# Performance work log

Measured on AMD Instinct MI355X. Metric: run time of the kernel, lower is better.

Reference implementation:

```python
import jax, jax.numpy as jnp
import numpy as np

B, C, H, W, K, NH = 4, 128, 64, 64, 7, 8
DH = C // NH          # per-head dim
PAD = (K - 1) // 2    # symmetric padding since K is odd


def setup_inputs() -> dict:
    key = jax.random.key(0)
    ks = jax.random.split(key, 9)
    s = 1.0 / np.sqrt(C)
    f32 = jnp.float32
    return {
        "x": jax.random.normal(ks[0], (B, C, H, W), f32),
        "wq": jax.random.normal(ks[1], (C, C), f32) * s,
        "bq": jax.random.normal(ks[2], (C,), f32) * 0.01,
        "wk": jax.random.normal(ks[3], (C, C), f32) * s,
        "bk": jax.random.normal(ks[4], (C,), f32) * 0.01,
        "wv": jax.random.normal(ks[5], (C, C), f32) * s,
        "bv": jax.random.normal(ks[6], (C,), f32) * 0.01,
        "pos_h": jax.random.normal(ks[7], (NH, K), f32) * 0.02,
        "pos_w": jax.random.normal(ks[8], (NH, K), f32) * 0.02,
    }


def _unfold(p):
    # p: [B,C,H+K-1,W+K-1] -> [B,C,H,W,K,K] (KxK neighborhood per pixel),
    # matching torch .unfold(2,K,1).unfold(3,K,1). Loop is over fixed kernel size only.
    p1 = jnp.stack([p[:, :, i:i + H, :] for i in range(K)], axis=-1)      # [B,C,H,W+K-1,K]
    return jnp.stack([p1[:, :, :, j:j + W, :] for j in range(K)], axis=-1)  # [B,C,H,W,K,K]


def reference(x, wq, bq, wk, bk, wv, bv, pos_h, pos_w):
    cx = x  # cx defaults to x in the original module
    pc = jnp.pad(cx, ((0, 0), (0, 0), (PAD, PAD), (PAD, PAD)))
    # 1x1 convs are pointwise channel mixes
    k = jnp.einsum('oc,bchw->bohw', wk, pc) + bk[None, :, None, None]
    v = jnp.einsum('oc,bchw->bohw', wv, pc) + bv[None, :, None, None]
    q = jnp.einsum('oc,bchw->bohw', wq, x) + bq[None, :, None, None]

    ku = _unfold(k).reshape(B, NH, DH, H, W, K, K)
    vu = _unfold(v).reshape(B, NH, DH, H, W, K, K)
    qh = q.reshape(B, NH, DH, H, W)

    # per-pixel logits over KxK neighborhood
    logits = jnp.einsum('bndhw,bndhwij->bnhwij', qh, ku)  # [B,NH,H,W,K,K]
    logits = logits + pos_h[None, :, None, None, :, None] + pos_w[None, :, None, None, None, :]

    weights = jax.nn.softmax(logits.reshape(B, NH, H, W, K * K), axis=-1)
    out = jnp.einsum('bnhwk,bndhwk->bndhw', weights, vu.reshape(B, NH, DH, H, W, K * K))
    return out.reshape(B, C, H, W)
```

## Files before the change

### kernel.cpp

```cpp
#include <hip/hip_runtime.h>
#include <cmath>

constexpr int Bn = 4, Cn = 128, Hn = 64, Wn = 64, Kn = 7, NHn = 8, DHn = 16, PADn = 3;
constexpr int HWn = Hn * Wn;
constexpr int TS = 16;
constexpr int HALO = TS + Kn - 1;
constexpr int DP = 20;
constexpr int SMEM_ELEMS = HALO * HALO * DP;

typedef float f32x4 __attribute__((ext_vector_type(4)));
typedef short short8 __attribute__((ext_vector_type(8)));
typedef unsigned int u32x4 __attribute__((ext_vector_type(4)));

__device__ __forceinline__ unsigned short f32_to_bf16_rne(float f) {
  unsigned u = __float_as_uint(f);
  unsigned r = u + 0x7fffu + ((u >> 16) & 1u);
  return (unsigned short)(r >> 16);
}
__device__ __forceinline__ float bf16_to_f32(unsigned short h) {
  return __uint_as_float(((unsigned)h) << 16);
}

__global__ __launch_bounds__(256)
void conv_w(const float* __restrict__ wq, const float* __restrict__ wk,
            const float* __restrict__ wv, unsigned short* __restrict__ Whl)
{
  const int mat = blockIdx.y;
  const float* W = (mat == 0) ? wq : (mat == 1) ? wk : wv;
  const int i = (blockIdx.x * 256 + threadIdx.x) * 4;
  const f32x4 v = *reinterpret_cast<const f32x4*>(W + i);
  unsigned short h[4], l[4];
#pragma unroll
  for (int j = 0; j < 4; ++j) {
    h[j] = f32_to_bf16_rne(v[j]);
    l[j] = f32_to_bf16_rne(v[j] - bf16_to_f32(h[j]));
  }
  unsigned short* base = Whl + (size_t)mat * 2 * 16384;
  unsigned int hw0 = h[0] | ((unsigned)h[1] << 16), hw1 = h[2] | ((unsigned)h[3] << 16);
  unsigned int lw0 = l[0] | ((unsigned)l[1] << 16), lw1 = l[2] | ((unsigned)l[3] << 16);
  *reinterpret_cast<uint2*>(base + i)          = make_uint2(hw0, hw1);
  *reinterpret_cast<uint2*>(base + 16384 + i)  = make_uint2(lw0, lw1);
}

__global__ __launch_bounds__(256)
void conv_xT(const float* __restrict__ x, unsigned short* __restrict__ xThl)
{
  __shared__ float sm[32][65];
  const int b   = blockIdx.z;
  const int c0g = blockIdx.y * 32;
  const int p0g = blockIdx.x * 64;
  const int t   = threadIdx.x;
  const float* xb = x + (size_t)b * Cn * HWn;

#pragma unroll
  for (int rep = 0; rep < 2; ++rep) {
    const int cl = rep * 16 + (t >> 4);
    const int pl = (t & 15) * 4;
    const f32x4 v = *reinterpret_cast<const f32x4*>(xb + (size_t)(c0g + cl) * HWn + p0g + pl);
    sm[cl][pl + 0] = v[0]; sm[cl][pl + 1] = v[1];
    sm[cl][pl + 2] = v[2]; sm[cl][pl + 3] = v[3];
  }
  __syncthreads();

  const int pl = t >> 2;
  const int c0 = (t & 3) * 8;
  u32x4 hw, lw;
#pragma unroll
  for (int j = 0; j < 4; ++j) {
    const float v0 = sm[c0 + 2 * j][pl];
    const float v1 = sm[c0 + 2 * j + 1][pl];
    const unsigned short h0 = f32_to_bf16_rne(v0);
    const unsigned short h1 = f32_to_bf16_rne(v1);
    const unsigned short l0 = f32_to_bf16_rne(v0 - bf16_to_f32(h0));
    const unsigned short l1 = f32_to_bf16_rne(v1 - bf16_to_f32(h1));
    hw[j] = h0 | ((unsigned)h1 << 16);
    lw[j] = l0 | ((unsigned)l1 << 16);
  }
  unsigned short* dst = xThl + (size_t)b * 2 * HWn * Cn + (size_t)(p0g + pl) * Cn + c0g + c0;
  *reinterpret_cast<u32x4*>(dst)             = hw;
  *reinterpret_cast<u32x4*>(dst + HWn * Cn)  = lw;
}

__global__ __launch_bounds__(64)
void qkv_mfma(const unsigned short* __restrict__ Whl,
              const unsigned short* __restrict__ xThl,
              const float* __restrict__ bq_, const float* __restrict__ bk_,
              const float* __restrict__ bv_,
              float* __restrict__ qo, float* __restrict__ ko, float* __restrict__ vo)
{
  const int z   = blockIdx.z;
  const int mat = z >> 2;
  const int b   = z & 3;
  const float* bias = (mat == 0) ? bq_ : (mat == 1) ? bk_ : bv_;
  float* y = ((mat == 0) ? qo : (mat == 1) ? ko : vo) + (size_t)b * Cn * HWn;

  const int lane = threadIdx.x;
  const int r    = lane & 15;
  const int quad = lane >> 4;
  const int mbase = blockIdx.y * 64;
  const int nbase = blockIdx.x * 64;

  const unsigned short* Wm = Whl  + (size_t)mat * 2 * Cn * Cn;
  const unsigned short* Xb = xThl + (size_t)b   * 2 * HWn * Cn;

  f32x4 acc[4][4] = {};

#pragma unroll
  for (int ks = 0; ks < 4; ++ks) {
    const int kk = ks * 32 + quad * 8;
    short8 Ah[4], Al[4], Bh[4], Bl[4];
#pragma unroll
    for (int mt = 0; mt < 4; ++mt) {
      const unsigned short* p = Wm + (size_t)(mbase + mt * 16 + r) * Cn + kk;
      Ah[mt] = *reinterpret_cast<const short8*>(p);
      Al[mt] = *reinterpret_cast<const short8*>(p + Cn * Cn);
    }
#pragma unroll
    for (int nt = 0; nt < 4; ++nt) {
      const unsigned short* p = Xb + (size_t)(nbase + nt * 16 + r) * Cn + kk;
      Bh[nt] = *reinterpret_cast<const short8*>(p);
      Bl[nt] = *reinterpret_cast<const short8*>(p + HWn * Cn);
    }
#pragma unroll
    for (int mt = 0; mt < 4; ++mt)
#pragma unroll
      for (int nt = 0; nt < 4; ++nt) {
        acc[mt][nt] = __builtin_amdgcn_mfma_f32_16x16x32_bf16(Ah[mt], Bh[nt], acc[mt][nt], 0, 0, 0);
        acc[mt][nt] = __builtin_amdgcn_mfma_f32_16x16x32_bf16(Ah[mt], Bl[nt], acc[mt][nt], 0, 0, 0);
        acc[mt][nt] = __builtin_amdgcn_mfma_f32_16x16x32_bf16(Al[mt], Bh[nt], acc[mt][nt], 0, 0, 0);
      }
  }

#pragma unroll
  for (int mt = 0; mt < 4; ++mt) {
#pragma unroll
    for (int reg = 0; reg < 4; ++reg) {
      const int o = mbase + mt * 16 + quad * 4 + reg;
      const float bi = bias[o];
#pragma unroll
      for (int nt = 0; nt < 4; ++nt)
        y[(size_t)o * HWn + nbase + nt * 16 + r] = acc[mt][nt][reg] + bi;
    }
  }
}

__global__ __launch_bounds__(256)
void sasa_attn(const float* __restrict__ q, const float* __restrict__ k,
               const float* __restrict__ v, const float* __restrict__ bk_,
               const float* __restrict__ bv_, const float* __restrict__ pos_h,
               const float* __restrict__ pos_w, float* __restrict__ out)
{
  extern __shared__ float smem[];
  float* ks = smem;
  float* vs = smem + SMEM_ELEMS;

  const int z  = blockIdx.z;
  const int b  = z >> 3;
  const int n  = z & 7;
  const int h0 = blockIdx.y * TS;
  const int w0 = blockIdx.x * TS;
  const int tid = threadIdx.x;
  const int tx = tid & 15;
  const int ty = tid >> 4;

  const int cbase = n * DHn;
  const size_t plane = (size_t)HWn;
  const float* kb = k + ((size_t)b * Cn + cbase) * plane;
  const float* vb = v + ((size_t)b * Cn + cbase) * plane;

  for (int idx = tid; idx < HALO * HALO * DHn; idx += 256) {
    const int d   = idx / (HALO * HALO);
    const int rem = idx - d * (HALO * HALO);
    const int hh  = rem / HALO;
    const int ww  = rem - hh * HALO;
    const int gh  = h0 + hh - PADn;
    const int gw  = w0 + ww - PADn;
    const bool inb = (gh >= 0) && (gh < Hn) && (gw >= 0) && (gw < Wn);
    const int lidx = (hh * HALO + ww) * DP + d;
    ks[lidx] = inb ? kb[(size_t)d * plane + gh * Wn + gw] : bk_[cbase + d];
    vs[lidx] = inb ? vb[(size_t)d * plane + gh * Wn + gw] : bv_[cbase + d];
  }

  const int h = h0 + ty, w = w0 + tx;
  const float* qb = q + ((size_t)b * Cn + cbase) * plane + (size_t)h * Wn + w;
  float qr[DHn];
#pragma unroll
  for (int d = 0; d < DHn; ++d) qr[d] = qb[(size_t)d * plane];

  __syncthreads();

  float logits[Kn * Kn];
#pragma unroll
  for (int i = 0; i < Kn; ++i) {
    const float ph = pos_h[n * Kn + i];
#pragma unroll
    for (int j = 0; j < Kn; ++j) {
      const float* kp = &ks[((ty + i) * HALO + (tx + j)) * DP];
      const float4 k0 = *reinterpret_cast<const float4*>(kp);
      const float4 k1 = *reinterpret_cast<const float4*>(kp + 4);
      const float4 k2 = *reinterpret_cast<const float4*>(kp + 8);
      const float4 k3 = *reinterpret_cast<const float4*>(kp + 12);
      float acc = qr[0] * k0.x;
      acc = fmaf(qr[1],  k0.y, acc);  acc = fmaf(qr[2],  k0.z, acc);
      acc = fmaf(qr[3],  k0.w, acc);  acc = fmaf(qr[4],  k1.x, acc);
      acc = fmaf(qr[5],  k1.y, acc);  acc = fmaf(qr[6],  k1.z, acc);
      acc = fmaf(qr[7],  k1.w, acc);  acc = fmaf(qr[8],  k2.x, acc);
      acc = fmaf(qr[9],  k2.y, acc);  acc = fmaf(qr[10], k2.z, acc);
      acc = fmaf(qr[11], k2.w, acc);  acc = fmaf(qr[12], k3.x, acc);
      acc = fmaf(qr[13], k3.y, acc);  acc = fmaf(qr[14], k3.z, acc);
      acc = fmaf(qr[15], k3.w, acc);
      logits[i * Kn + j] = acc + ph + pos_w[n * Kn + j];
    }
  }

  float mx = -1e30f;
#pragma unroll
  for (int t = 0; t < Kn * Kn; ++t) mx = fmaxf(mx, logits[t]);
  float sum = 0.0f;
#pragma unroll
  for (int t = 0; t < Kn * Kn; ++t) {
    const float e = __expf(logits[t] - mx);
    logits[t] = e;
    sum += e;
  }
  const float inv = 1.0f / sum;

  float o[DHn] = {};
#pragma unroll
  for (int i = 0; i < Kn; ++i) {
#pragma unroll
    for (int j = 0; j < Kn; ++j) {
      const float wt = logits[i * Kn + j];
      const float* vp = &vs[((ty + i) * HALO + (tx + j)) * DP];
      const float4 v0 = *reinterpret_cast<const float4*>(vp);
      const float4 v1 = *reinterpret_cast<const float4*>(vp + 4);
      const float4 v2 = *reinterpret_cast<const float4*>(vp + 8);
      const float4 v3 = *reinterpret_cast<const float4*>(vp + 12);
      o[0]  = fmaf(wt, v0.x, o[0]);   o[1]  = fmaf(wt, v0.y, o[1]);
      o[2]  = fmaf(wt, v0.z, o[2]);   o[3]  = fmaf(wt, v0.w, o[3]);
      o[4]  = fmaf(wt, v1.x, o[4]);   o[5]  = fmaf(wt, v1.y, o[5]);
      o[6]  = fmaf(wt, v1.z, o[6]);   o[7]  = fmaf(wt, v1.w, o[7]);
      o[8]  = fmaf(wt, v2.x, o[8]);   o[9]  = fmaf(wt, v2.y, o[9]);
      o[10] = fmaf(wt, v2.z, o[10]);  o[11] = fmaf(wt, v2.w, o[11]);
      o[12] = fmaf(wt, v3.x, o[12]);  o[13] = fmaf(wt, v3.y, o[13]);
      o[14] = fmaf(wt, v3.z, o[14]);  o[15] = fmaf(wt, v3.w, o[15]);
    }
  }

  float* ob = out + ((size_t)b * Cn + cbase) * plane + (size_t)h * Wn + w;
#pragma unroll
  for (int d = 0; d < DHn; ++d) ob[(size_t)d * plane] = o[d] * inv;
}

extern "C" void kernel_launch(void* const* d_in, const int* in_sizes, int n_in,
                              void* d_out, int out_size, void* d_ws, size_t ws_size,
                              hipStream_t stream) {
  const float* x     = (const float*)d_in[0];
  const float* wq    = (const float*)d_in[1];
  const float* bq    = (const float*)d_in[2];
  const float* wk    = (const float*)d_in[3];
  const float* bk    = (const float*)d_in[4];
  const float* wv    = (const float*)d_in[5];
  const float* bv    = (const float*)d_in[6];
  const float* pos_h = (const float*)d_in[7];
  const float* pos_w = (const float*)d_in[8];
  float* out = (float*)d_out;

  const size_t tensor_elems = (size_t)Bn * Cn * HWn;
  float* q = (float*)d_ws;
  float* k = q + tensor_elems;
  float* v = k + tensor_elems;
  unsigned short* Whl  = (unsigned short*)(v + tensor_elems);
  unsigned short* xThl = Whl + (size_t)3 * 2 * Cn * Cn;

  dim3 gw(16, 3, 1);
  conv_w<<<gw, 256, 0, stream>>>(wq, wk, wv, Whl);

  dim3 gx(HWn / 64, Cn / 32, Bn);
  conv_xT<<<gx, 256, 0, stream>>>(x, xThl);

  dim3 g1(HWn / 64, Cn / 64, 3 * Bn);
  qkv_mfma<<<g1, 64, 0, stream>>>(Whl, xThl, bq, bk, bv, q, k, v);

  dim3 g2(Wn / TS, Hn / TS, Bn * NHn);
  const size_t smem_bytes = 2 * SMEM_ELEMS * sizeof(float);
  sasa_attn<<<g2, 256, smem_bytes, stream>>>(q, k, v, bk, bv, pos_h, pos_w, out);
}
```

Baseline: 132.9 us.

## Store K/V as bf16 in head-pixel-major layout and merge prep kernels

The QKV GEMM epilogue now writes Q as fp32 and K/V as bf16 in a [B,NH,HW,DH] layout. This lets the attention kernel fill its halo tiles with 16-byte vector loads instead of strided scalar gathers, and halves the K/V global traffic and shared-memory footprint. The weight and x conversion kernels are merged into one launch to save a launch. Storing K/V in bf16 lowers their precision, which may hurt accuracy against the fp32 reference.

```diff
diff --git a/kernel.cpp b/kernel.cpp
--- a/kernel.cpp
+++ b/kernel.cpp
@@ -5,12 +5,15 @@
 constexpr int HWn = Hn * Wn;
 constexpr int TS = 16;
 constexpr int HALO = TS + Kn - 1;
-constexpr int DP = 20;
-constexpr int SMEM_ELEMS = HALO * HALO * DP;
+constexpr int NPIX = HALO * HALO;
+constexpr int PSTRIDE_U16 = 24;
+constexpr int PSTRIDE_U32 = 12;
 
 typedef float f32x4 __attribute__((ext_vector_type(4)));
 typedef short short8 __attribute__((ext_vector_type(8)));
 typedef unsigned int u32x4 __attribute__((ext_vector_type(4)));
+typedef unsigned short u16x4 __attribute__((ext_vector_type(4)));
+typedef unsigned short u16x8 __attribute__((ext_vector_type(8)));
 
 __device__ __forceinline__ unsigned short f32_to_bf16_rne(float f) {
   unsigned u = __float_as_uint(f);
@@ -20,36 +23,41 @@
 __device__ __forceinline__ float bf16_to_f32(unsigned short h) {
   return __uint_as_float(((unsigned)h) << 16);
 }
+__device__ __forceinline__ float bflo(unsigned u) { return __uint_as_float(u << 16); }
+__device__ __forceinline__ float bfhi(unsigned u) { return __uint_as_float(u & 0xffff0000u); }
 
 __global__ __launch_bounds__(256)
-void conv_w(const float* __restrict__ wq, const float* __restrict__ wk,
-            const float* __restrict__ wv, unsigned short* __restrict__ Whl)
+void prep(const float* __restrict__ x,
+          const float* __restrict__ wq, const float* __restrict__ wk,
+          const float* __restrict__ wv,
+          unsigned short* __restrict__ Whl, unsigned short* __restrict__ xThl)
 {
-  const int mat = blockIdx.y;
-  const float* W = (mat == 0) ? wq : (mat == 1) ? wk : wv;
-  const int i = (blockIdx.x * 256 + threadIdx.x) * 4;
-  const f32x4 v = *reinterpret_cast<const f32x4*>(W + i);
-  unsigned short h[4], l[4];
-#pragma unroll
-  for (int j = 0; j < 4; ++j) {
-    h[j] = f32_to_bf16_rne(v[j]);
-    l[j] = f32_to_bf16_rne(v[j] - bf16_to_f32(h[j]));
-  }
-  unsigned short* base = Whl + (size_t)mat * 2 * 16384;
-  unsigned int hw0 = h[0] | ((unsigned)h[1] << 16), hw1 = h[2] | ((unsigned)h[3] << 16);
-  unsigned int lw0 = l[0] | ((unsigned)l[1] << 16), lw1 = l[2] | ((unsigned)l[3] << 16);
-  *reinterpret_cast<uint2*>(base + i)          = make_uint2(hw0, hw1);
-  *reinterpret_cast<uint2*>(base + 16384 + i)  = make_uint2(lw0, lw1);
-}
-
-__global__ __launch_bounds__(256)
-void conv_xT(const float* __restrict__ x, unsigned short* __restrict__ xThl)
-{
+  const int t = threadIdx.x;
+  if (blockIdx.z == 4) {
+    if (blockIdx.y != 0 || blockIdx.x >= 48) return;
+    const int mat = blockIdx.x >> 4;
+    const int chunk = blockIdx.x & 15;
+    const float* W = (mat == 0) ? wq : (mat == 1) ? wk : wv;
+    const int i = (chunk * 256 + t) * 4;
+    const f32x4 v = *reinterpret_cast<const f32x4*>(W + i);
+    unsigned short h[4], l[4];
+#pragma unroll
+    for (int j = 0; j < 4; ++j) {
+      h[j] = f32_to_bf16_rne(v[j]);
+      l[j] = f32_to_bf16_rne(v[j] - bf16_to_f32(h[j]));
+    }
+    unsigned short* base = Whl + (size_t)mat * 2 * 16384;
+    *reinterpret_cast<uint2*>(base + i) =
+        make_uint2(h[0] | ((unsigned)h[1] << 16), h[2] | ((unsigned)h[3] << 16));
+    *reinterpret_cast<uint2*>(base + 16384 + i) =
+        make_uint2(l[0] | ((unsigned)l[1] << 16), l[2] | ((unsigned)l[3] << 16));
+    return;
+  }
+
   __shared__ float sm[32][65];
   const int b   = blockIdx.z;
   const int c0g = blockIdx.y * 32;
   const int p0g = blockIdx.x * 64;
-  const int t   = threadIdx.x;
   const float* xb = x + (size_t)b * Cn * HWn;
 
 #pragma unroll
@@ -77,8 +85,8 @@
     lw[j] = l0 | ((unsigned)l1 << 16);
   }
   unsigned short* dst = xThl + (size_t)b * 2 * HWn * Cn + (size_t)(p0g + pl) * Cn + c0g + c0;
-  *reinterpret_cast<u32x4*>(dst)             = hw;
-  *reinterpret_cast<u32x4*>(dst + HWn * Cn)  = lw;
+  *reinterpret_cast<u32x4*>(dst)            = hw;
+  *reinterpret_cast<u32x4*>(dst + HWn * Cn) = lw;
 }
 
 __global__ __launch_bounds__(64)
@@ -86,13 +94,13 @@
               const unsigned short* __restrict__ xThl,
               const float* __restrict__ bq_, const float* __restrict__ bk_,
               const float* __restrict__ bv_,
-              float* __restrict__ qo, float* __restrict__ ko, float* __restrict__ vo)
+              float* __restrict__ qo, unsigned short* __restrict__ kbf,
+              unsigned short* __restrict__ vbf)
 {
   const int z   = blockIdx.z;
   const int mat = z >> 2;
   const int b   = z & 3;
   const float* bias = (mat == 0) ? bq_ : (mat == 1) ? bk_ : bv_;
-  float* y = ((mat == 0) ? qo : (mat == 1) ? ko : vo) + (size_t)b * Cn * HWn;
 
   const int lane = threadIdx.x;
   const int r    = lane & 15;
@@ -133,26 +141,34 @@
 
 #pragma unroll
   for (int mt = 0; mt < 4; ++mt) {
-#pragma unroll
-    for (int reg = 0; reg < 4; ++reg) {
-      const int o = mbase + mt * 16 + quad * 4 + reg;
-      const float bi = bias[o];
-#pragma unroll
-      for (int nt = 0; nt < 4; ++nt)
-        y[(size_t)o * HWn + nbase + nt * 16 + r] = acc[mt][nt][reg] + bi;
+    const int n = blockIdx.y * 4 + mt;
+    const f32x4 b4 = *reinterpret_cast<const f32x4*>(bias + mbase + mt * 16 + quad * 4);
+#pragma unroll
+    for (int nt = 0; nt < 4; ++nt) {
+      const int p = nbase + nt * 16 + r;
+      const size_t off = ((size_t)((b * NHn + n) * HWn + p)) * DHn + quad * 4;
+      f32x4 val = acc[mt][nt] + b4;
+      if (mat == 0) {
+        *reinterpret_cast<f32x4*>(qo + off) = val;
+      } else {
+        unsigned short* y = (mat == 1) ? kbf : vbf;
+        u16x4 pk;
+        pk[0] = f32_to_bf16_rne(val[0]); pk[1] = f32_to_bf16_rne(val[1]);
+        pk[2] = f32_to_bf16_rne(val[2]); pk[3] = f32_to_bf16_rne(val[3]);
+        *reinterpret_cast<u16x4*>(y + off) = pk;
+      }
     }
   }
 }
 
 __global__ __launch_bounds__(256)
-void sasa_attn(const float* __restrict__ q, const float* __restrict__ k,
-               const float* __restrict__ v, const float* __restrict__ bk_,
+void sasa_attn(const float* __restrict__ q, const unsigned short* __restrict__ kbf,
+               const unsigned short* __restrict__ vbf, const float* __restrict__ bk_,
                const float* __restrict__ bv_, const float* __restrict__ pos_h,
                const float* __restrict__ pos_w, float* __restrict__ out)
 {
-  extern __shared__ float smem[];
-  float* ks = smem;
-  float* vs = smem + SMEM_ELEMS;
+  __shared__ __align__(16) unsigned short ksm[NPIX * PSTRIDE_U16];
+  __shared__ __align__(16) unsigned short vsm[NPIX * PSTRIDE_U16];
 
   const int z  = blockIdx.z;
   const int b  = z >> 3;
@@ -162,32 +178,57 @@
   const int tid = threadIdx.x;
   const int tx = tid & 15;
   const int ty = tid >> 4;
-
   const int cbase = n * DHn;
-  const size_t plane = (size_t)HWn;
-  const float* kb = k + ((size_t)b * Cn + cbase) * plane;
-  const float* vb = v + ((size_t)b * Cn + cbase) * plane;
-
-  for (int idx = tid; idx < HALO * HALO * DHn; idx += 256) {
-    const int d   = idx / (HALO * HALO);
-    const int rem = idx - d * (HALO * HALO);
-    const int hh  = rem / HALO;
-    const int ww  = rem - hh * HALO;
-    const int gh  = h0 + hh - PADn;
-    const int gw  = w0 + ww - PADn;
+
+  const unsigned short* kb = kbf + ((size_t)(b * NHn + n) * HWn) * DHn;
+  const unsigned short* vb = vbf + ((size_t)(b * NHn + n) * HWn) * DHn;
+
+  u16x8 kb0, kb1, vb0, vb1;
+#pragma unroll
+  for (int j = 0; j < 8; ++j) {
+    kb0[j] = f32_to_bf16_rne(bk_[cbase + j]);
+    kb1[j] = f32_to_bf16_rne(bk_[cbase + 8 + j]);
+    vb0[j] = f32_to_bf16_rne(bv_[cbase + j]);
+    vb1[j] = f32_to_bf16_rne(bv_[cbase + 8 + j]);
+  }
+
+  for (int c = tid; c < NPIX * 2; c += 256) {
+    const int pix  = c >> 1;
+    const int half = c & 1;
+    const int hh = pix / HALO;
+    const int ww = pix - hh * HALO;
+    const int gh = h0 + hh - PADn;
+    const int gw = w0 + ww - PADn;
     const bool inb = (gh >= 0) && (gh < Hn) && (gw >= 0) && (gw < Wn);
-    const int lidx = (hh * HALO + ww) * DP + d;
-    ks[lidx] = inb ? kb[(size_t)d * plane + gh * Wn + gw] : bk_[cbase + d];
-    vs[lidx] = inb ? vb[(size_t)d * plane + gh * Wn + gw] : bv_[cbase + d];
+    u16x8 kd, vd;
+    if (inb) {
+      const size_t src = ((size_t)(gh * Wn + gw)) * DHn + half * 8;
+      kd = *reinterpret_cast<const u16x8*>(kb + src);
+      vd = *reinterpret_cast<const u16x8*>(vb + src);
+    } else {
+      kd = half ? kb1 : kb0;
+      vd = half ? vb1 : vb0;
+    }
+    const int dst = pix * PSTRIDE_U16 + half * 8;
+    *reinterpret_cast<u16x8*>(ksm + dst) = kd;
+    *reinterpret_cast<u16x8*>(vsm + dst) = vd;
   }
 
   const int h = h0 + ty, w = w0 + tx;
-  const float* qb = q + ((size_t)b * Cn + cbase) * plane + (size_t)h * Wn + w;
+  const int p = h * Wn + w;
+  const float* qp = q + ((size_t)(b * NHn + n) * HWn + p) * DHn;
   float qr[DHn];
 #pragma unroll
-  for (int d = 0; d < DHn; ++d) qr[d] = qb[(size_t)d * plane];
+  for (int j = 0; j < 4; ++j) {
+    const f32x4 t4 = *reinterpret_cast<const f32x4*>(qp + j * 4);
+    qr[j * 4 + 0] = t4[0]; qr[j * 4 + 1] = t4[1];
+    qr[j * 4 + 2] = t4[2]; qr[j * 4 + 3] = t4[3];
+  }
 
   __syncthreads();
+
+  const unsigned* ksu = reinterpret_cast<const unsigned*>(ksm);
+  const unsigned* vsu = reinterpret_cast<const unsigned*>(vsm);
 
   float logits[Kn * Kn];
 #pragma unroll
@@ -195,20 +236,18 @@
     const float ph = pos_h[n * Kn + i];
 #pragma unroll
     for (int j = 0; j < Kn; ++j) {
-      const float* kp = &ks[((ty + i) * HALO + (tx + j)) * DP];
-      const float4 k0 = *reinterpret_cast<const float4*>(kp);
-      const float4 k1 = *reinterpret_cast<const float4*>(kp + 4);
-      const float4 k2 = *reinterpret_cast<const float4*>(kp + 8);
-      const float4 k3 = *reinterpret_cast<const float4*>(kp + 12);
-      float acc = qr[0] * k0.x;
-      acc = fmaf(qr[1],  k0.y, acc);  acc = fmaf(qr[2],  k0.z, acc);
-      acc = fmaf(qr[3],  k0.w, acc);  acc = fmaf(qr[4],  k1.x, acc);
-      acc = fmaf(qr[5],  k1.y, acc);  acc = fmaf(qr[6],  k1.z, acc);
-      acc = fmaf(qr[7],  k1.w, acc);  acc = fmaf(qr[8],  k2.x, acc);
-      acc = fmaf(qr[9],  k2.y, acc);  acc = fmaf(qr[10], k2.z, acc);
-      acc = fmaf(qr[11], k2.w, acc);  acc = fmaf(qr[12], k3.x, acc);
-      acc = fmaf(qr[13], k3.y, acc);  acc = fmaf(qr[14], k3.z, acc);
-      acc = fmaf(qr[15], k3.w, acc);
+      const int base = ((ty + i) * HALO + (tx + j)) * PSTRIDE_U32;
+      const u32x4 a = *reinterpret_cast<const u32x4*>(ksu + base);
+      const u32x4 c = *reinterpret_cast<const u32x4*>(ksu + base + 4);
+      float acc = qr[0] * bflo(a[0]);
+      acc = fmaf(qr[1],  bfhi(a[0]), acc);
+      acc = fmaf(qr[2],  bflo(a[1]), acc);  acc = fmaf(qr[3],  bfhi(a[1]), acc);
+      acc = fmaf(qr[4],  bflo(a[2]), acc);  acc = fmaf(qr[5],  bfhi(a[2]), acc);
+      acc = fmaf(qr[6],  bflo(a[3]), acc);  acc = fmaf(qr[7],  bfhi(a[3]), acc);
+      acc = fmaf(qr[8],  bflo(c[0]), acc);  acc = fmaf(qr[9],  bfhi(c[0]), acc);
+      acc = fmaf(qr[10], bflo(c[1]), acc);  acc = fmaf(qr[11], bfhi(c[1]), acc);
+      acc = fmaf(qr[12], bflo(c[2]), acc);  acc = fmaf(qr[13], bfhi(c[2]), acc);
+      acc = fmaf(qr[14], bflo(c[3]), acc);  acc = fmaf(qr[15], bfhi(c[3]), acc);
       logits[i * Kn + j] = acc + ph + pos_w[n * Kn + j];
     }
   }
@@ -231,25 +270,23 @@
 #pragma unroll
     for (int j = 0; j < Kn; ++j) {
       const float wt = logits[i * Kn + j];
-      const float* vp = &vs[((ty + i) * HALO + (tx + j)) * DP];
-      const float4 v0 = *reinterpret_cast<const float4*>(vp);
-      const float4 v1 = *reinterpret_cast<const float4*>(vp + 4);
-      const float4 v2 = *reinterpret_cast<const float4*>(vp + 8);
-      const float4 v3 = *reinterpret_cast<const float4*>(vp + 12);
-      o[0]  = fmaf(wt, v0.x, o[0]);   o[1]  = fmaf(wt, v0.y, o[1]);
-      o[2]  = fmaf(wt, v0.z, o[2]);   o[3]  = fmaf(wt, v0.w, o[3]);
-      o[4]  = fmaf(wt, v1.x, o[4]);   o[5]  = fmaf(wt, v1.y, o[5]);
-      o[6]  = fmaf(wt, v1.z, o[6]);   o[7]  = fmaf(wt, v1.w, o[7]);
-      o[8]  = fmaf(wt, v2.x, o[8]);   o[9]  = fmaf(wt, v2.y, o[9]);
-      o[10] = fmaf(wt, v2.z, o[10]);  o[11] = fmaf(wt, v2.w, o[11]);
-      o[12] = fmaf(wt, v3.x, o[12]);  o[13] = fmaf(wt, v3.y, o[13]);
-      o[14] = fmaf(wt, v3.z, o[14]);  o[15] = fmaf(wt, v3.w, o[15]);
-    }
-  }
-
-  float* ob = out + ((size_t)b * Cn + cbase) * plane + (size_t)h * Wn + w;
-#pragma unroll
-  for (int d = 0; d < DHn; ++d) ob[(size_t)d * plane] = o[d] * inv;
+      const int base = ((ty + i) * HALO + (tx + j)) * PSTRIDE_U32;
+      const u32x4 a = *reinterpret_cast<const u32x4*>(vsu + base);
+      const u32x4 c = *reinterpret_cast<const u32x4*>(vsu + base + 4);
+      o[0]  = fmaf(wt, bflo(a[0]), o[0]);   o[1]  = fmaf(wt, bfhi(a[0]), o[1]);
+      o[2]  = fmaf(wt, bflo(a[1]), o[2]);   o[3]  = fmaf(wt, bfhi(a[1]), o[3]);
+      o[4]  = fmaf(wt, bflo(a[2]), o[4]);   o[5]  = fmaf(wt, bfhi(a[2]), o[5]);
+      o[6]  = fmaf(wt, bflo(a[3]), o[6]);   o[7]  = fmaf(wt, bfhi(a[3]), o[7]);
+      o[8]  = fmaf(wt, bflo(c[0]), o[8]);   o[9]  = fmaf(wt, bfhi(c[0]), o[9]);
+      o[10] = fmaf(wt, bflo(c[1]), o[10]);  o[11] = fmaf(wt, bfhi(c[1]), o[11]);
+      o[12] = fmaf(wt, bflo(c[2]), o[12]);  o[13] = fmaf(wt, bfhi(c[2]), o[13]);
+      o[14] = fmaf(wt, bflo(c[3]), o[14]);  o[15] = fmaf(wt, bfhi(c[3]), o[15]);
+    }
+  }
+
+  float* ob = out + ((size_t)(b * Cn + cbase)) * HWn + p;
+#pragma unroll
+  for (int d = 0; d < DHn; ++d) ob[(size_t)d * HWn] = o[d] * inv;
 }
 
 extern "C" void kernel_launch(void* const* d_in, const int* in_sizes, int n_in,
@@ -267,22 +304,18 @@
   float* out = (float*)d_out;
 
   const size_t tensor_elems = (size_t)Bn * Cn * HWn;
-  float* q = (float*)d_ws;
-  float* k = q + tensor_elems;
-  float* v = k + tensor_elems;
-  unsigned short* Whl  = (unsigned short*)(v + tensor_elems);
+  float*          q    = (float*)d_ws;
+  unsigned short* kbf  = (unsigned short*)(q + tensor_elems);
+  unsigned short* vbf  = kbf + tensor_elems;
+  unsigned short* Whl  = vbf + tensor_elems;
   unsigned short* xThl = Whl + (size_t)3 * 2 * Cn * Cn;
 
-  dim3 gw(16, 3, 1);
-  conv_w<<<gw, 256, 0, stream>>>(wq, wk, wv, Whl);
-
-  dim3 gx(HWn / 64, Cn / 32, Bn);
-  conv_xT<<<gx, 256, 0, stream>>>(x, xThl);
+  dim3 gp(HWn / 64, Cn / 32, Bn + 1);
+  prep<<<gp, 256, 0, stream>>>(x, wq, wk, wv, Whl, xThl);
 
   dim3 g1(HWn / 64, Cn / 64, 3 * Bn);
-  qkv_mfma<<<g1, 64, 0, stream>>>(Whl, xThl, bq, bk, bv, q, k, v);
+  qkv_mfma<<<g1, 64, 0, stream>>>(Whl, xThl, bq, bk, bv, q, kbf, vbf);
 
   dim3 g2(Wn / TS, Hn / TS, Bn * NHn);
-  const size_t smem_bytes = 2 * SMEM_ELEMS * sizeof(float);
-  sasa_attn<<<g2, 256, smem_bytes, stream>>>(q, k, v, bk, bv, pos_h, pos_w, out);
-}
+  sasa_attn<<<g2, 256, 0, stream>>>(q, kbf, vbf, bk, bv, pos_h, pos_w, out);
+}
```

Result: faster. 110.8 us (-16.6%).
